# Performance work log

Hardware: AMD Instinct MI355X
Metric: run time of the kernel (lower is better)

## Reference

```python
import jax, jax.numpy as jnp
import numpy as np

N_EMBD = 1024
N_HEAD = 16
HEAD_DIM = N_EMBD // N_HEAD

def setup_inputs() -> dict:
    key = jax.random.key(0)
    ks = jax.random.split(key, 9)
    B, T, C = 2, 2048, N_EMBD
    s = 1.0 / np.sqrt(C)
    x = jax.random.normal(ks[0], (B, T, C), dtype=jnp.float32)
    Wk = jax.random.normal(ks[1], (C, C), dtype=jnp.float32) * s
    bk = jnp.zeros((C,), dtype=jnp.float32)
    Wq = jax.random.normal(ks[2], (C, C), dtype=jnp.float32) * s
    bq = jnp.zeros((C,), dtype=jnp.float32)
    Wv = jax.random.normal(ks[3], (C, C), dtype=jnp.float32) * s
    bv = jnp.zeros((C,), dtype=jnp.float32)
    Wp = jax.random.normal(ks[4], (C, C), dtype=jnp.float32) * s
    bp = jnp.zeros((C,), dtype=jnp.float32)
    return {"x": x, "Wq": Wq, "bq": bq, "Wk": Wk, "bk": bk, "Wv": Wv, "bv": bv, "Wp": Wp, "bp": bp}

def reference(x, Wq, bq, Wk, bk, Wv, bv, Wp, bp):
    B, T, C = x.shape
    H, D = N_HEAD, HEAD_DIM
    # QKV projections (torch Linear: x @ W.T + b; here W is stored as (in,out))
    q = (x @ Wq + bq).reshape(B, T, H, D).transpose(0, 2, 1, 3)  # [B,H,T,D]
    k = (x @ Wk + bk).reshape(B, T, H, D).transpose(0, 2, 1, 3)
    v = (x @ Wv + bv).reshape(B, T, H, D).transpose(0, 2, 1, 3)
    att = jnp.einsum('bhtd,bhsd->bhts', q, k) / jnp.sqrt(jnp.float32(D))
    causal = jnp.tril(jnp.ones((T, T), dtype=bool))
    att = jnp.where(causal, att, jnp.float32(-jnp.inf))
    att = jax.nn.softmax(att, axis=-1)
    y = jnp.einsum('bhts,bhsd->bhtd', att, v)  # [B,H,T,D]
    y = y.transpose(0, 2, 1, 3).reshape(B, T, C)
    return y @ Wp + bp
```

## Files before the change

kernel.cpp:

```cpp
#include <hip/hip_runtime.h>
#include <cstdint>

typedef __attribute__((ext_vector_type(4))) short s16x4;
typedef __attribute__((ext_vector_type(8))) short s16x8;
typedef __attribute__((ext_vector_type(4))) float f32x4;
typedef __attribute__((ext_vector_type(16))) float f32x16;

#define L2E 1.44269504088896340736f

__device__ __forceinline__ short f2bf(float f) {
  union { float f; unsigned u; } v; v.f = f;
  unsigned r = (v.u + 0x7fffu + ((v.u >> 16) & 1u)) >> 16;
  return (short)r;
}

__device__ __forceinline__ float xhalf_f(float x) {
  union { float f; unsigned u; } a; a.f = x;
  auto r = __builtin_amdgcn_permlane32_swap(a.u, a.u, false, false);
  union { unsigned u; float f; } b;
  b.u = (threadIdx.x & 32) ? r[0] : r[1];
  return b.f;
}

typedef const __attribute__((address_space(1))) unsigned int* gas_p;
typedef __attribute__((address_space(3))) unsigned int* las_p;
__device__ __forceinline__ void stage16(const void* g, void* l) {
  __builtin_amdgcn_global_load_lds((gas_p)(uintptr_t)g,
                                   (las_p)(unsigned int)(uintptr_t)l, 16, 0, 0);
}

__global__ __launch_bounds__(256) void prepass(const float* __restrict__ W0,
                                               const float* __restrict__ W1,
                                               const float* __restrict__ W2,
                                               const float* __restrict__ W3,
                                               short* __restrict__ wdst,
                                               const float* __restrict__ x,
                                               short* __restrict__ xb) {
  const int z = blockIdx.z;
  const int t = threadIdx.x;
  if (z >= 4) {
    int i = ((z - 4) * 256 + blockIdx.y * 16 + blockIdx.x) * 256 + t;
    const f32x4* p = (const f32x4*)x + (size_t)i * 2;
    f32x4 a = p[0], b = p[1];
    s16x8 o;
    o[0] = f2bf(a[0]); o[1] = f2bf(a[1]); o[2] = f2bf(a[2]); o[3] = f2bf(a[3]);
    o[4] = f2bf(b[0]); o[5] = f2bf(b[1]); o[6] = f2bf(b[2]); o[7] = f2bf(b[3]);
    *((s16x8*)xb + i) = o;
    return;
  }
  __shared__ float tile[64][65];
  const float* in = (z == 0) ? W0 : (z == 1) ? W1 : (z == 2) ? W2 : W3;
  short* out = wdst + (size_t)z * 1048576;
  const int bi = blockIdx.y, bj = blockIdx.x;
  const int c = t & 63, r0 = t >> 6;
#pragma unroll
  for (int i = 0; i < 16; i++) {
    int r = r0 + i * 4;
    tile[r][c] = in[(size_t)(bi * 64 + r) * 1024 + bj * 64 + c];
  }
  __syncthreads();
#pragma unroll
  for (int i = 0; i < 16; i++) {
    int r = r0 + i * 4;
    out[(size_t)(bj * 64 + r) * 1024 + bi * 64 + c] = f2bf(tile[c][r]);
  }
}

template <int EPI, int BM, int BN>
__global__ __launch_bounds__((BM / 64) * (BN / 64) * 64) void gemm_bt(
    const short* __restrict__ A, const short* __restrict__ B, int N, int K,
    const float* __restrict__ b0, const float* __restrict__ b1,
    const float* __restrict__ b2, short* __restrict__ o0, short* __restrict__ o1,
    short* __restrict__ o2, float* __restrict__ ofp) {
  constexpr int T = (BM / 64) * (BN / 64) * 64;
  constexpr int AR = BM * 8 / T;
  constexpr int BR = BN * 8 / T;
  __shared__ short As[2][BM * 32];
  __shared__ short Bs[2][BN * 32];
  const int tid = threadIdx.x;
  const int lane = tid & 63;
  const int wave = tid >> 6;
  const int wr = wave / (BN / 64), wc = wave % (BN / 64);
  const int l15 = lane & 15, l4 = lane >> 4;
  const int id = blockIdx.x + gridDim.x * blockIdx.y;
  const int cpx = gridDim.x >> 3;
  const int xcd = id & 7, sub = id >> 3;
  const int m0 = (sub / cpx) * BM;
  const int n0 = (xcd * cpx + sub % cpx) * BN;
  const short* Ab = A + (size_t)m0 * K;
  const short* Bb = B + (size_t)n0 * K;
  f32x4 acc[4][4];
#pragma unroll
  for (int i = 0; i < 4; i++)
#pragma unroll
    for (int j = 0; j < 4; j++) acc[i][j] = (f32x4){0.f, 0.f, 0.f, 0.f};

  const int lq = tid & 3, lr = tid >> 2;
  int soffA[AR], goffA[AR];
#pragma unroll
  for (int i = 0; i < AR; i++) {
    const int flat = i * (T / 4) + lr;
    const int p = flat / BM, r = flat % BM;
    soffA[i] = p * BM * 32 + r * 32 + lq * 8;
    goffA[i] = r * K + p * 32 + lq * 8;
  }
  int soffB[BR], goffB[BR];
#pragma unroll
  for (int j = 0; j < BR; j++) {
    const int flat = j * (T / 4) + lr;
    const int p = flat / BN, r = flat % BN;
    soffB[j] = p * BN * 32 + r * 32 + lq * 8;
    goffB[j] = r * K + p * 32 + lq * 8;
  }

  for (int k0 = 0; k0 < K; k0 += 64) {
#pragma unroll
    for (int i = 0; i < AR; i++)
      stage16(Ab + (size_t)(goffA[i] + k0), (short*)As + soffA[i]);
#pragma unroll
    for (int j = 0; j < BR; j++)
      stage16(Bb + (size_t)(goffB[j] + k0), (short*)Bs + soffB[j]);
    __syncthreads();
#pragma unroll
    for (int ks = 0; ks < 2; ks++) {
      s16x8 af[4], bfr[4];
#pragma unroll
      for (int i = 0; i < 4; i++) {
        af[i] = *(const s16x8*)((short*)As + ks * BM * 32 + (wr * 64 + i * 16 + l15) * 32 + l4 * 8);
        bfr[i] = *(const s16x8*)((short*)Bs + ks * BN * 32 + (wc * 64 + i * 16 + l15) * 32 + l4 * 8);
      }
#pragma unroll
      for (int mi = 0; mi < 4; mi++)
#pragma unroll
        for (int ni = 0; ni < 4; ni++)
          acc[mi][ni] = __builtin_amdgcn_mfma_f32_16x16x32_bf16(af[mi], bfr[ni],
                                                                acc[mi][ni], 0, 0, 0);
    }
    __syncthreads();
  }

#pragma unroll
  for (int ni = 0; ni < 4; ni++) {
    const int col = n0 + wc * 64 + ni * 16 + l15;
    if (EPI == 1) {
      const float bias = b0[col];
#pragma unroll
      for (int mi = 0; mi < 4; mi++)
#pragma unroll
        for (int r = 0; r < 4; r++) {
          int row = m0 + wr * 64 + mi * 16 + l4 * 4 + r;
          ofp[(size_t)row * N + col] = acc[mi][ni][r] + bias;
        }
    } else {
      const float* bp; short* dst; int c1; int isV = 0; float scl = 1.0f;
      if (col < 1024) { bp = b0; dst = o0; c1 = col; scl = 0.125f * L2E; }
      else if (col < 2048) { bp = b1; dst = o1; c1 = col - 1024; }
      else { bp = b2; dst = o2; c1 = col - 2048; isV = 1; }
      const float bias = bp[c1];
      const int h = c1 >> 6, d = c1 & 63;
      if (isV) {
#pragma unroll
        for (int mi = 0; mi < 4; mi++) {
          int t0 = m0 + wr * 64 + mi * 16 + l4 * 4;
          int bb = t0 >> 11, t = t0 & 2047;
          s16x4 ov;
#pragma unroll
          for (int r = 0; r < 4; r++) ov[r] = f2bf(acc[mi][ni][r] + bias);
          *(s16x4*)(dst + (size_t)((bb * 16 + h) * 64 + d) * 2048 + t) = ov;
        }
      } else {
#pragma unroll
        for (int mi = 0; mi < 4; mi++)
#pragma unroll
          for (int r = 0; r < 4; r++) {
            int row = m0 + wr * 64 + mi * 16 + l4 * 4 + r;
            int bb = row >> 11, t = row & 2047;
            float v = (acc[mi][ni][r] + bias) * scl;
            dst[(size_t)((bb * 16 + h) * 2048 + t) * 64 + d] = f2bf(v);
          }
      }
    }
  }
}

__global__ __launch_bounds__(128) void attn_v8(const short* __restrict__ Q,
                                               const short* __restrict__ K,
                                               const short* __restrict__ Vt,
                                               short* __restrict__ Y) {
  __shared__ short Ks[2][64 * 64];
  __shared__ short Vs[3][64 * 64];
  const int bh = blockIdx.x;
  const int y = blockIdx.y;
  const int g = y >> 3, r_ = y & 7;
  const int qbase = (g << 3) | ((g & 1) ? (7 - r_) : r_);
  const int qt = (qbase + ((bh & 3) << 3)) & 31;
  const int tid = threadIdx.x, lane = tid & 63, wave = tid >> 6;
  const int q31 = lane & 31, hi = lane >> 5;
  const short* Qp = Q + (size_t)bh * 2048 * 64;
  const short* Kp = K + (size_t)bh * 2048 * 64;
  const short* Vp = Vt + (size_t)bh * 64 * 2048;
  const int qrow = qt * 64 + wave * 32 + q31;
  const int nt = qt + 1;
  const int cx = q31 & 7;

  s16x8 qf[4];
#pragma unroll
  for (int s = 0; s < 4; s++)
    qf[s] = *(const s16x8*)(Qp + (size_t)qrow * 64 + s * 16 + hi * 8);

  f32x16 accA, accB, Z;
#pragma unroll
  for (int i = 0; i < 16; i++) { accA[i] = 0.f; accB[i] = 0.f; Z[i] = 0.f; }
  float l = 0.f;

  const int srow = tid >> 3, sch = tid & 7;
  int sdst[4], koff[4], voff[4];
#pragma unroll
  for (int i = 0; i < 4; i++) {
    const int r = srow + i * 16;
    const int sc = sch ^ (r & 7);
    sdst[i] = r * 64 + sch * 8;
    koff[i] = r * 64 + sc * 8;
    voff[i] = r * 2048 + sc * 8;
  }
  const short* kst = Kp;
  const short* vst = Vp;
  int rd0[4];
#pragma unroll
  for (int s = 0; s < 4; s++) rd0[s] = q31 * 64 + (((2 * s + hi) ^ cx) << 3);

  short* kA = &Ks[0][0]; short* kB = &Ks[1][0];
  short* vP = &Vs[2][0]; short* vC = &Vs[0][0]; short* vN = &Vs[1][0];

#pragma unroll
  for (int i = 0; i < 4; i++) {
    stage16(kst + koff[i], kA + sdst[i]);
    stage16(vst + voff[i], vC + sdst[i]);
  }
  kst += 4096; vst += 64;

#define STAGE_NEXT(COND)                                                       \
  if (COND) {                                                                  \
    _Pragma("unroll") for (int i_ = 0; i_ < 4; i_++) {                         \
      stage16(kst + koff[i_], kB + sdst[i_]);                                  \
      stage16(vst + voff[i_], vN + sdst[i_]);                                  \
    }                                                                          \
    kst += 4096; vst += 64;                                                    \
  }

#define QK(S0, S1)                                                             \
  {                                                                            \
    s16x8 kf0_[4], kf1_[4];                                                    \
    _Pragma("unroll") for (int s_ = 0; s_ < 4; s_++) {                         \
      kf0_[s_] = *(const s16x8*)(kA + rd0[s_]);                                \
      kf1_[s_] = *(const s16x8*)(kA + rd0[s_] + 2048);                         \
    }                                                                          \
    __builtin_amdgcn_s_setprio(1);                                             \
    S0 = __builtin_amdgcn_mfma_f32_32x32x16_bf16(kf0_[0], qf[0], Z, 0, 0, 0);  \
    S1 = __builtin_amdgcn_mfma_f32_32x32x16_bf16(kf1_[0], qf[0], Z, 0, 0, 0);  \
    _Pragma("unroll") for (int s_ = 1; s_ < 4; s_++) {                         \
      S0 = __builtin_amdgcn_mfma_f32_32x32x16_bf16(kf0_[s_], qf[s_], S0, 0, 0, 0); \
      S1 = __builtin_amdgcn_mfma_f32_32x32x16_bf16(kf1_[s_], qf[s_], S1, 0, 0, 0); \
    }                                                                          \
    __builtin_amdgcn_s_setprio(0);                                             \
  }

#define SMPV_BODY(S0, S1)                                                      \
  {                                                                            \
    float rsum_ = 0.f;                                                         \
    _Pragma("unroll") for (int r2_ = 0; r2_ < 16; r2_++) {                     \
      float p_ = __builtin_amdgcn_exp2f(S0[r2_]);                              \
      S0[r2_] = p_; rsum_ += p_;                                               \
    }                                                                          \
    _Pragma("unroll") for (int r2_ = 0; r2_ < 16; r2_++) {                     \
      float p_ = __builtin_amdgcn_exp2f(S1[r2_]);                              \
      S1[r2_] = p_; rsum_ += p_;                                               \
    }                                                                          \
    l += rsum_;                                                                \
    unsigned pk0_[8], pk1_[8];                                                 \
    _Pragma("unroll") for (int j_ = 0; j_ < 8; j_++) {                         \
      unsigned u_;                                                             \
      float a0_ = S0[2 * j_], a1_ = S0[2 * j_ + 1];                            \
      asm("v_cvt_pk_bf16_f32 %0, %1, %2" : "=v"(u_) : "v"(a0_), "v"(a1_));     \
      pk0_[j_] = u_;                                                           \
      float b0_ = S1[2 * j_], b1_ = S1[2 * j_ + 1];                            \
      asm("v_cvt_pk_bf16_f32 %0, %1, %2" : "=v"(u_) : "v"(b0_), "v"(b1_));     \
      pk1_[j_] = u_;                                                           \
    }                                                                          \
    _Pragma("unroll") for (int s_ = 0; s_ < 4; s_++) {                         \
      const unsigned* pk_ = (s_ < 2) ? pk0_ : pk1_;                            \
      const int b_ = 4 * (s_ & 1);                                             \
      auto rA_ = __builtin_amdgcn_permlane32_swap(pk_[b_ + 0], pk_[b_ + 2], false, false); \
      auto rB_ = __builtin_amdgcn_permlane32_swap(pk_[b_ + 1], pk_[b_ + 3], false, false); \
      union { unsigned u[4]; s16x8 v; } fr_;                                   \
      fr_.u[0] = rA_[0]; fr_.u[1] = rB_[0]; fr_.u[2] = rA_[1]; fr_.u[3] = rB_[1]; \
      s16x8 vf0_ = *(const s16x8*)(vP + rd0[s_]);                              \
      s16x8 vf1_ = *(const s16x8*)(vP + rd0[s_] + 2048);                       \
      __builtin_amdgcn_s_setprio(1);                                           \
      accA = __builtin_amdgcn_mfma_f32_32x32x16_bf16(vf0_, fr_.v, accA, 0, 0, 0); \
      accB = __builtin_amdgcn_mfma_f32_32x32x16_bf16(vf1_, fr_.v, accB, 0, 0, 0); \
      __builtin_amdgcn_s_setprio(0);                                           \
    }                                                                          \
  }

#define SMPV_MASK(S0, S1)                                                      \
  {                                                                            \
    const int k0_ = (nt - 1) * 64;                                             \
    _Pragma("unroll") for (int r2_ = 0; r2_ < 16; r2_++) {                     \
      int kvr_ = k0_ + (r2_ & 3) + 8 * (r2_ >> 2) + 4 * hi;                    \
      if (kvr_ > qrow) S0[r2_] = -__builtin_inff();                            \
      if (kvr_ + 32 > qrow) S1[r2_] = -__builtin_inff();                       \
    }                                                                          \
    SMPV_BODY(S0, S1)                                                          \
  }

#define ROT()                                                                  \
  {                                                                            \
    short* t_ = kA; kA = kB; kB = t_;                                          \
    t_ = vP; vP = vC; vC = vN; vN = t_;                                        \
  }

  f32x16 sA0, sA1, sB0, sB1;
  __syncthreads();
  STAGE_NEXT(nt > 1)
  QK(sA0, sA1)
  ROT()
  int t = 1;
  for (; t + 1 < nt; t += 2) {
    __syncthreads();
    STAGE_NEXT(t + 1 < nt)
    QK(sB0, sB1)
    SMPV_BODY(sA0, sA1)
    ROT()
    __syncthreads();
    STAGE_NEXT(t + 2 < nt)
    QK(sA0, sA1)
    SMPV_BODY(sB0, sB1)
    ROT()
  }
  if (t < nt) {
    __syncthreads();
    QK(sB0, sB1)
    SMPV_BODY(sA0, sA1)
    ROT()
    SMPV_MASK(sB0, sB1)
  } else {
    SMPV_MASK(sA0, sA1)
  }
#undef STAGE_NEXT
#undef QK
#undef SMPV_BODY
#undef SMPV_MASK
#undef ROT

  const int b_ = bh >> 4, h_ = bh & 15;
  const float lt = l + xhalf_f(l);
  const float invl = 1.f / lt;
  const size_t base = ((size_t)b_ * 2048 + qrow) * 1024 + h_ * 64;
#pragma unroll
  for (int gg = 0; gg < 4; gg++) {
    s16x4 o0, o1;
#pragma unroll
    for (int e = 0; e < 4; e++) {
      o0[e] = f2bf(accA[4 * gg + e] * invl);
      o1[e] = f2bf(accB[4 * gg + e] * invl);
    }
    *(s16x4*)(Y + base + 8 * gg + 4 * hi) = o0;
    *(s16x4*)(Y + base + 32 + 8 * gg + 4 * hi) = o1;
  }
}

extern "C" void kernel_launch(void* const* d_in, const int* in_sizes, int n_in,
                              void* d_out, int out_size, void* d_ws, size_t ws_size,
                              hipStream_t stream) {
  const float* x = (const float*)d_in[0];
  const float* Wq = (const float*)d_in[1];
  const float* bq = (const float*)d_in[2];
  const float* Wk = (const float*)d_in[3];
  const float* bk = (const float*)d_in[4];
  const float* Wv = (const float*)d_in[5];
  const float* bv = (const float*)d_in[6];
  const float* Wp = (const float*)d_in[7];
  const float* bp = (const float*)d_in[8];
  float* out = (float*)d_out;
  char* ws = (char*)d_ws;

  short* xb    = (short*)(ws + 0);
  short* WqkvT = (short*)(ws + 8388608);
  short* WpT   = (short*)(ws + 14680064);
  short* Qb    = (short*)(ws + 16777216);
  short* Kb    = (short*)(ws + 25165824);
  short* Vtb   = (short*)(ws + 33554432);
  short* Yb    = xb;

  prepass<<<dim3(16, 16, 12), 256, 0, stream>>>(Wq, Wk, Wv, Wp, WqkvT, x, xb);
  gemm_bt<0, 256, 128><<<dim3(24, 16), 512, 0, stream>>>(xb, WqkvT, 3072, 1024,
                                                         bq, bk, bv, Qb, Kb, Vtb,
                                                         nullptr);
  attn_v8<<<dim3(32, 32), 128, 0, stream>>>(Qb, Kb, Vtb, Yb);
  gemm_bt<1, 64, 128><<<dim3(8, 64), 128, 0, stream>>>(Yb, WpT, 1024, 1024, bp,
                                                       nullptr, nullptr, nullptr,
                                                       nullptr, nullptr, out);
}
```

Before: 108.3 us.

## Triple-buffer GEMM LDS staging with async prefetch and enlarge output-projection tile

Replaces the single-stage load/sync/compute loop in the bf16 GEMM with a three-buffer ring. Global-to-LDS loads for tile k+2 are issued before the compute on tile k, and an explicit vmcnt wait plus one barrier per iteration replace the two __syncthreads. This is meant to hide global load latency behind MFMA work. The output projection GEMM also switches from 64x128 tiles with 128 threads to 128x128 tiles with 256 threads, which halves the grid. The cost is more LDS per block, which may lower occupancy, and the QKV GEMM now uses about 147KB of LDS.

```diff
diff --git a/kernel.cpp b/kernel.cpp
--- a/kernel.cpp
+++ b/kernel.cpp
@@ -66,29 +66,28 @@
   }
 }
 
-template <int EPI, int BM, int BN>
-__global__ __launch_bounds__((BM / 64) * (BN / 64) * 64) void gemm_bt(
+template <int EPI, int BM>
+__global__ __launch_bounds__(BM * 2) void gemm_bt(
     const short* __restrict__ A, const short* __restrict__ B, int N, int K,
     const float* __restrict__ b0, const float* __restrict__ b1,
     const float* __restrict__ b2, short* __restrict__ o0, short* __restrict__ o1,
     short* __restrict__ o2, float* __restrict__ ofp) {
-  constexpr int T = (BM / 64) * (BN / 64) * 64;
+  constexpr int T = BM * 2;
   constexpr int AR = BM * 8 / T;
-  constexpr int BR = BN * 8 / T;
-  __shared__ short As[2][BM * 32];
-  __shared__ short Bs[2][BN * 32];
+  constexpr int BR = 128 * 8 / T;
+  constexpr int LOADS = AR + BR;
+  constexpr int BUFB = (BM + 128) * 64;
+  __shared__ short L[3 * BUFB];
   const int tid = threadIdx.x;
   const int lane = tid & 63;
   const int wave = tid >> 6;
-  const int wr = wave / (BN / 64), wc = wave % (BN / 64);
+  const int wr = wave >> 1, wc = wave & 1;
   const int l15 = lane & 15, l4 = lane >> 4;
   const int id = blockIdx.x + gridDim.x * blockIdx.y;
   const int cpx = gridDim.x >> 3;
   const int xcd = id & 7, sub = id >> 3;
   const int m0 = (sub / cpx) * BM;
-  const int n0 = (xcd * cpx + sub % cpx) * BN;
-  const short* Ab = A + (size_t)m0 * K;
-  const short* Bb = B + (size_t)n0 * K;
+  const int n0 = (xcd * cpx + sub % cpx) * 128;
   f32x4 acc[4][4];
 #pragma unroll
   for (int i = 0; i < 4; i++)
@@ -108,26 +107,42 @@
 #pragma unroll
   for (int j = 0; j < BR; j++) {
     const int flat = j * (T / 4) + lr;
-    const int p = flat / BN, r = flat % BN;
-    soffB[j] = p * BN * 32 + r * 32 + lq * 8;
+    const int p = flat >> 7, r = flat & 127;
+    soffB[j] = BM * 64 + p * 4096 + r * 32 + lq * 8;
     goffB[j] = r * K + p * 32 + lq * 8;
   }
 
-  for (int k0 = 0; k0 < K; k0 += 64) {
-#pragma unroll
-    for (int i = 0; i < AR; i++)
-      stage16(Ab + (size_t)(goffA[i] + k0), (short*)As + soffA[i]);
-#pragma unroll
-    for (int j = 0; j < BR; j++)
-      stage16(Bb + (size_t)(goffB[j] + k0), (short*)Bs + soffB[j]);
-    __syncthreads();
+  const short* Asrc = A + (size_t)m0 * K;
+  const short* Bsrc = B + (size_t)n0 * K;
+  short* bufC = L;
+  short* bufN = L + BUFB;
+  short* bufS = L + 2 * BUFB;
+
+#define GSTAGE(BUF)                                                            \
+  {                                                                            \
+    _Pragma("unroll") for (int i_ = 0; i_ < AR; i_++)                          \
+        stage16(Asrc + goffA[i_], (BUF) + soffA[i_]);                          \
+    _Pragma("unroll") for (int j_ = 0; j_ < BR; j_++)                          \
+        stage16(Bsrc + goffB[j_], (BUF) + soffB[j_]);                          \
+    Asrc += 64; Bsrc += 64;                                                    \
+  }
+
+  GSTAGE(bufC)
+  GSTAGE(bufN)
+  asm volatile("s_waitcnt vmcnt(%0)" ::"i"(LOADS) : "memory");
+  __builtin_amdgcn_s_barrier();
+  __builtin_amdgcn_sched_barrier(0);
+
+  const int NK = K >> 6;
+  for (int kt = 0; kt < NK; kt++) {
+    if (kt + 2 < NK) GSTAGE(bufS)
 #pragma unroll
     for (int ks = 0; ks < 2; ks++) {
       s16x8 af[4], bfr[4];
 #pragma unroll
       for (int i = 0; i < 4; i++) {
-        af[i] = *(const s16x8*)((short*)As + ks * BM * 32 + (wr * 64 + i * 16 + l15) * 32 + l4 * 8);
-        bfr[i] = *(const s16x8*)((short*)Bs + ks * BN * 32 + (wc * 64 + i * 16 + l15) * 32 + l4 * 8);
+        af[i] = *(const s16x8*)(bufC + ks * BM * 32 + (wr * 64 + i * 16 + l15) * 32 + l4 * 8);
+        bfr[i] = *(const s16x8*)(bufC + BM * 64 + ks * 4096 + (wc * 64 + i * 16 + l15) * 32 + l4 * 8);
       }
 #pragma unroll
       for (int mi = 0; mi < 4; mi++)
@@ -136,8 +151,18 @@
           acc[mi][ni] = __builtin_amdgcn_mfma_f32_16x16x32_bf16(af[mi], bfr[ni],
                                                                 acc[mi][ni], 0, 0, 0);
     }
-    __syncthreads();
-  }
+    if (kt + 1 < NK) {
+      if (kt + 2 < NK) {
+        asm volatile("s_waitcnt vmcnt(%0)" ::"i"(LOADS) : "memory");
+      } else {
+        asm volatile("s_waitcnt vmcnt(0)" ::: "memory");
+      }
+      __builtin_amdgcn_s_barrier();
+      __builtin_amdgcn_sched_barrier(0);
+      short* t_ = bufC; bufC = bufN; bufN = bufS; bufS = t_;
+    }
+  }
+#undef GSTAGE
 
 #pragma unroll
   for (int ni = 0; ni < 4; ni++) {
@@ -394,11 +419,10 @@
   short* Yb    = xb;
 
   prepass<<<dim3(16, 16, 12), 256, 0, stream>>>(Wq, Wk, Wv, Wp, WqkvT, x, xb);
-  gemm_bt<0, 256, 128><<<dim3(24, 16), 512, 0, stream>>>(xb, WqkvT, 3072, 1024,
-                                                         bq, bk, bv, Qb, Kb, Vtb,
-                                                         nullptr);
+  gemm_bt<0, 256><<<dim3(24, 16), 512, 0, stream>>>(xb, WqkvT, 3072, 1024, bq, bk,
+                                                    bv, Qb, Kb, Vtb, nullptr);
   attn_v8<<<dim3(32, 32), 128, 0, stream>>>(Qb, Kb, Vtb, Yb);
-  gemm_bt<1, 64, 128><<<dim3(8, 64), 128, 0, stream>>>(Yb, WpT, 1024, 1024, bp,
-                                                       nullptr, nullptr, nullptr,
-                                                       nullptr, nullptr, out);
-}
+  gemm_bt<1, 128><<<dim3(8, 32), 256, 0, stream>>>(Yb, WpT, 1024, 1024, bp, nullptr,
+                                                   nullptr, nullptr, nullptr,
+                                                   nullptr, out);
+}
```

Result: no change. 110.3 us (+1.9%).
